# Optimization experiments

Measured on AMD Instinct MI355X. Metric: run time of the kernel, lower is better.

## Reference

```python
import jax, jax.numpy as jnp
import numpy as np

TOPK = 0.1  # fraction of h*w spatial positions, from __init__ default


def setup_inputs() -> dict:
    key = jax.random.key(0)
    x = jax.random.normal(key, (32, 256, 56, 56), dtype=jnp.float32)
    return {"x": x}


def reference(x) -> jnp.ndarray:
    # Faithful translation of TopKLayer.sparse_hw (including its quirky
    # comparison of ascending *ranks* against the spatial *index* of the
    # k-th largest element, exactly as the torch code does).
    n, c, h, w = x.shape
    k = int(max(1, TOPK * h * w))  # topk_keep_num = 313 for 56x56
    x_r = x.reshape(n * c, h * w)              # (nc, hw)
    abs_x = jnp.abs(x_r)
    # ranks[i, j] = ascending rank of abs_x[i, j] within row i
    ranks = jnp.argsort(jnp.argsort(abs_x, axis=1), axis=1)
    # spatial index of the k-th largest |x| in each row
    thr_idx = jax.lax.top_k(abs_x, k)[1][:, -1]  # (nc,)
    mask = (ranks < thr_idx[:, None]).reshape(n, c, h, w)
    return x * mask.astype(x.dtype)
```

## Files before the change

kernel.cpp:

```cpp
#include <hip/hip_runtime.h>
#include <stdint.h>


#define HW    3136
#define NT    256
#define KSEL  313u
#define CAP   320u
#define CAP2  64u
#define M31   0x7fffffffu
#define SENT  0xFFFFFFFFu

#define O_H    0
#define O_CAND 1088
#define O_HC   1408
#define O_TINY 1664
#define LDSW   1728

__device__ __forceinline__ unsigned wscan_incl(unsigned v) {
    const int lane = threadIdx.x & 63;
#pragma unroll
    for (int d = 1; d < 64; d <<= 1) {
        unsigned o = __shfl_up(v, d, 64);
        if (lane >= d) v += o;
    }
    return v;
}

__device__ __forceinline__ unsigned bcast_first(unsigned flag, unsigned val) {
    unsigned long long bal = __ballot(flag != 0);
    if (!bal) return 0u;
    return __shfl(val, __ffsll(bal) - 1, 64);
}

__device__ __forceinline__ void hadd(unsigned* h, unsigned b) {
    const unsigned w = b >> 1;
    atomicAdd(&h[w + (w >> 4)], (b & 1) ? 0x10000u : 1u);
}

template <bool fromTop>
__device__ unsigned wave_finish(unsigned* lds, unsigned m1, unsigned cnt) {
    const int lane = threadIdx.x & 63;
    unsigned* cand = lds + O_CAND;
    unsigned* hc   = lds + O_HC;
    unsigned* tiny = lds + O_TINY;
    if (m1 == 0) return 0u;
    if (cnt > CAP) return SENT;
    for (unsigned i = lane; i < cnt; i += 64) atomicAdd(&hc[cand[i] >> 24], 1u);
    unsigned hh[4];
#pragma unroll
    for (int i = 0; i < 4; ++i) hh[i] = hc[4 * lane + i];
    const unsigned s4 = hh[0] + hh[1] + hh[2] + hh[3];
    unsigned run2 = wscan_incl(s4) - s4;
    unsigned packed2 = 0;
#pragma unroll
    for (int i = 0; i < 4; ++i) {
        if (fromTop) {
            const unsigned suf = cnt - run2 - hh[i];
            if (suf < m1 && m1 <= suf + hh[i])
                packed2 = ((unsigned)(4 * lane + i) << 16) | (m1 - suf);
        } else {
            if (run2 < m1 && m1 <= run2 + hh[i])
                packed2 = ((unsigned)(4 * lane + i) << 16) | (m1 - run2);
        }
        run2 += hh[i];
    }
    packed2 = bcast_first(packed2, packed2);
    if (packed2 == 0) return 0u;
    const unsigned b2 = packed2 >> 16;
    const unsigned m2 = packed2 & 0xFFFFu;
    unsigned tc = 0;
    for (unsigned i = lane; i < cnt; i += 64) tc += ((cand[i] >> 24) == b2);
    const unsigned tincl = wscan_incl(tc);
    const unsigned c2 = __shfl((int)tincl, 63, 64);
    if (c2 > CAP2) return SENT;
    unsigned tpos = tincl - tc;
    for (unsigned i = lane; i < cnt; i += 64) {
        const unsigned cw = cand[i];
        if ((cw >> 24) == b2) tiny[tpos++] = cw;
    }
    unsigned hitf = 0, resv = 0;
    if ((unsigned)lane < c2) {
        const unsigned ci = tiny[lane];
        const unsigned di = fromTop ? (ci ^ 0xFFFu) : ci;
        unsigned r = 1;
        for (unsigned j = 0; j < c2; ++j) {
            const unsigned dj = fromTop ? (tiny[j] ^ 0xFFFu) : tiny[j];
            if (fromTop ? (dj > di) : (dj < di)) r++;
        }
        if (r == m2) { hitf = 1; resv = ci; }
    }
    return bcast_first(hitf, resv);
}

template <bool fromTop>
__device__ void block_fallback(const unsigned* __restrict__ gx,
                               unsigned b0, unsigned m1, unsigned* res) {
    const int t = threadIdx.x;
    for (int j = t; j < HW; j += NT) {
        const unsigned k = gx[j] & M31;
        if ((k >> 20) != b0) continue;
        unsigned Ci = ((k & 0xFFFFFu) << 12) | (unsigned)j;
        if (fromTop) Ci ^= 0xFFFu;
        unsigned r = 1;
        for (int j2 = 0; j2 < HW; ++j2) {
            const unsigned k2 = gx[j2] & M31;
            if ((k2 >> 20) != b0) continue;
            unsigned Cj = ((k2 & 0xFFFFFu) << 12) | (unsigned)j2;
            if (fromTop) Cj ^= 0xFFFu;
            if (fromTop ? (Cj > Ci) : (Cj < Ci)) r++;
        }
        if (r == m1) res[0] = ((k & 0xFFFFFu) << 12) | (unsigned)j;
    }
}

extern "C" __global__ void __launch_bounds__(NT, 6)
topk_kernel(const float* __restrict__ x, float* __restrict__ out) {
    __shared__ unsigned lds[LDSW];
    __shared__ unsigned s_warp[4];
    __shared__ unsigned s_b[4];

    const int t = threadIdx.x;
    const int lane = t & 63;
    const int wid = t >> 6;
    const size_t row = blockIdx.x;
    const uint4* __restrict__ xin = (const uint4*)(x + row * HW);
    uint4* __restrict__ xo = (uint4*)(out + row * HW);
    const unsigned* __restrict__ gx = (const unsigned*)xin;
    const uint4 z4 = make_uint4(0u, 0u, 0u, 0u);
    const bool tail = (t < 16);

    uint4 v0 = xin[t];
    uint4 v1 = xin[t + NT];
    uint4 v2 = xin[t + 2 * NT];
    uint4 vt = tail ? xin[768 + t] : z4;
    asm volatile("" : "+v"(v0.x), "+v"(v0.y), "+v"(v0.z), "+v"(v0.w));
    asm volatile("" : "+v"(v1.x), "+v"(v1.y), "+v"(v1.z), "+v"(v1.w));
    asm volatile("" : "+v"(v2.x), "+v"(v2.y), "+v"(v2.z), "+v"(v2.w));
    asm volatile("" : "+v"(vt.x), "+v"(vt.y), "+v"(vt.z), "+v"(vt.w));

    {
        uint4* h4 = (uint4*)(lds + O_H);
        h4[t] = z4;
        if (tail) h4[NT + t] = z4;
    }
    __syncthreads();

    hadd(lds, (v0.x & M31) >> 20); hadd(lds, (v0.y & M31) >> 20);
    hadd(lds, (v0.z & M31) >> 20); hadd(lds, (v0.w & M31) >> 20);
    hadd(lds, (v1.x & M31) >> 20); hadd(lds, (v1.y & M31) >> 20);
    hadd(lds, (v1.z & M31) >> 20); hadd(lds, (v1.w & M31) >> 20);
    hadd(lds, (v2.x & M31) >> 20); hadd(lds, (v2.y & M31) >> 20);
    hadd(lds, (v2.z & M31) >> 20); hadd(lds, (v2.w & M31) >> 20);
    if (tail) {
        hadd(lds, (vt.x & M31) >> 20); hadd(lds, (vt.y & M31) >> 20);
        hadd(lds, (vt.z & M31) >> 20); hadd(lds, (vt.w & M31) >> 20);
    }
    __syncthreads();

    unsigned cpk[4];
    {
        const unsigned a0 = 4u * (unsigned)t + ((unsigned)t >> 2);
#pragma unroll
        for (int j = 0; j < 4; ++j) cpk[j] = lds[O_H + a0 + j];
    }
    unsigned ssum = 0;
#pragma unroll
    for (int j = 0; j < 4; ++j) ssum += (cpk[j] & 0xFFFFu) + (cpk[j] >> 16);
    const unsigned Si = wscan_incl(ssum);
    if (lane == 63) s_warp[wid] = Si;
    __syncthreads();

    unsigned cross = 0;
    for (int w2 = 0; w2 < wid; ++w2) cross += s_warp[w2];
    const unsigned base = cross + Si - ssum;
    {
        unsigned run = base;
#pragma unroll
        for (int j = 0; j < 4; ++j) {
            const unsigned lo = cpk[j] & 0xFFFFu, hi = cpk[j] >> 16;
            unsigned suf = HW - run - lo;
            if (suf < KSEL && KSEL <= suf + lo) { s_b[0] = 8u * t + 2u * j; s_b[1] = KSEL - suf; }
            run += lo;
            suf = HW - run - hi;
            if (suf < KSEL && KSEL <= suf + hi) { s_b[0] = 8u * t + 2u * j + 1u; s_b[1] = KSEL - suf; }
            run += hi;
        }
    }
    if (t == 0) s_b[3] = 0;
    lds[O_HC + t] = 0;
    __syncthreads();

    auto compact_regs = [&](unsigned b0) {
        auto cput = [&](unsigned wv, unsigned idx) {
            const unsigned k = wv & M31;
            if ((k >> 20) == b0) {
                const unsigned p = atomicAdd(&s_b[3], 1u);
                if (p < CAP) lds[O_CAND + p] = ((k & 0xFFFFFu) << 12) | idx;
            }
        };
        unsigned i0 = 4u * (unsigned)t;
        cput(v0.x, i0); cput(v0.y, i0 + 1u); cput(v0.z, i0 + 2u); cput(v0.w, i0 + 3u);
        i0 = 4u * (unsigned)(t + NT);
        cput(v1.x, i0); cput(v1.y, i0 + 1u); cput(v1.z, i0 + 2u); cput(v1.w, i0 + 3u);
        i0 = 4u * (unsigned)(t + 2 * NT);
        cput(v2.x, i0); cput(v2.y, i0 + 1u); cput(v2.z, i0 + 2u); cput(v2.w, i0 + 3u);
        if (tail) {
            i0 = 4u * (unsigned)(768 + t);
            cput(vt.x, i0); cput(vt.y, i0 + 1u); cput(vt.z, i0 + 2u); cput(vt.w, i0 + 3u);
        }
    };
    const unsigned b0A = s_b[0];
    const unsigned m1A = s_b[1];
    compact_regs(b0A);
    __syncthreads();

    if (wid == 0) {
        const unsigned r = wave_finish<true>(lds, m1A, s_b[3]);
        if (lane == 0) s_b[2] = r;
    }
    __syncthreads();
    unsigned compA = s_b[2];
    if (compA == SENT) {
        block_fallback<true>(gx, b0A, m1A, &s_b[2]);
        __syncthreads();
        compA = s_b[2];
    }
    const unsigned tIdx = compA & 0xFFFu;

    {
        unsigned run = base;
#pragma unroll
        for (int j = 0; j < 4; ++j) {
            const unsigned lo = cpk[j] & 0xFFFFu, hi = cpk[j] >> 16;
            if (run < tIdx && tIdx <= run + lo) { s_b[0] = 8u * t + 2u * j; s_b[1] = tIdx - run; }
            run += lo;
            if (run < tIdx && tIdx <= run + hi) { s_b[0] = 8u * t + 2u * j + 1u; s_b[1] = tIdx - run; }
            run += hi;
        }
    }
    if (t == 0) {
        s_b[3] = 0;
        if (tIdx == 0) { s_b[0] = 0; s_b[1] = 0; }
    }
    lds[O_HC + t] = 0;
    __syncthreads();

    const unsigned b0B = s_b[0];
    const unsigned m1B = s_b[1];
    compact_regs(b0B);
    __syncthreads();

    if (wid == 0) {
        const unsigned r = wave_finish<false>(lds, m1B, s_b[3]);
        if (lane == 0) s_b[2] = r;
    }
    __syncthreads();
    unsigned compB = s_b[2];
    if (compB == SENT) {
        block_fallback<false>(gx, b0B, m1B, &s_b[2]);
        __syncthreads();
        compB = s_b[2];
    }
    const unsigned KB = (b0B << 20) | (compB >> 12);
    const unsigned eB = compB & 0xFFFu;

    {
        auto msk = [&](unsigned wv, unsigned idx) -> unsigned {
            const unsigned k = wv & M31;
            return (k < KB || (k == KB && idx <= eB)) ? wv : 0u;
        };
        uint4 o;
        unsigned i0 = 4u * (unsigned)t;
        o.x = msk(v0.x, i0); o.y = msk(v0.y, i0 + 1u);
        o.z = msk(v0.z, i0 + 2u); o.w = msk(v0.w, i0 + 3u);
        xo[t] = o;
        i0 = 4u * (unsigned)(t + NT);
        o.x = msk(v1.x, i0); o.y = msk(v1.y, i0 + 1u);
        o.z = msk(v1.z, i0 + 2u); o.w = msk(v1.w, i0 + 3u);
        xo[t + NT] = o;
        i0 = 4u * (unsigned)(t + 2 * NT);
        o.x = msk(v2.x, i0); o.y = msk(v2.y, i0 + 1u);
        o.z = msk(v2.z, i0 + 2u); o.w = msk(v2.w, i0 + 3u);
        xo[t + 2 * NT] = o;
        if (tail) {
            i0 = 4u * (unsigned)(768 + t);
            o.x = msk(vt.x, i0); o.y = msk(vt.y, i0 + 1u);
            o.z = msk(vt.z, i0 + 2u); o.w = msk(vt.w, i0 + 3u);
            xo[768 + t] = o;
        }
    }
}

extern "C" void kernel_launch(void* const* d_in, const int* in_sizes, int n_in,
                              void* d_out, int out_size, void* d_ws, size_t ws_size,
                              hipStream_t stream) {
    const float* x = (const float*)d_in[0];
    float* out = (float*)d_out;
    const int rows = in_sizes[0] / HW;
    topk_kernel<<<dim3(rows), dim3(NT), 0, stream>>>(x, out);
}
```

Baseline: 70.04 us.

## Stage row in LDS and halve block size to 128 threads

The block shrinks from 256 to 128 threads, and the whole 3136-element row is copied into shared memory instead of being held in registers. The compaction, fallback and final masking passes then read values from LDS rather than registers or global memory, and the histogram prefix scan now handles 16 bins per thread. The aim is to cut register pressure per thread and keep the fallback path from re-reading global memory. The cost is about 17 KB of LDS per block, fewer waves per block, and extra LDS traffic in every pass, which may reduce latency hiding for a bandwidth-bound kernel.

Result: slower. 74.77 us (+6.8%).

```diff
diff --git a/kernel.cpp b/kernel.cpp
--- a/kernel.cpp
+++ b/kernel.cpp
@@ -3,18 +3,20 @@
 
 
 #define HW    3136
-#define NT    256
+#define NW4   784
+#define NT    128
 #define KSEL  313u
 #define CAP   320u
 #define CAP2  64u
 #define M31   0x7fffffffu
 #define SENT  0xFFFFFFFFu
 
-#define O_H    0
-#define O_CAND 1088
-#define O_HC   1408
-#define O_TINY 1664
-#define LDSW   1728
+#define O_X    0
+#define O_H    3136
+#define O_CAND 3136
+#define O_HC   3520
+#define O_TINY 3776
+#define LDSW   4224
 
 __device__ __forceinline__ unsigned wscan_incl(unsigned v) {
     const int lane = threadIdx.x & 63;
@@ -93,17 +95,17 @@
 }
 
 template <bool fromTop>
-__device__ void block_fallback(const unsigned* __restrict__ gx,
-                               unsigned b0, unsigned m1, unsigned* res) {
+__device__ void block_fallback(const unsigned* sx, unsigned b0, unsigned m1,
+                               unsigned* res) {
     const int t = threadIdx.x;
     for (int j = t; j < HW; j += NT) {
-        const unsigned k = gx[j] & M31;
+        const unsigned k = sx[j] & M31;
         if ((k >> 20) != b0) continue;
         unsigned Ci = ((k & 0xFFFFFu) << 12) | (unsigned)j;
         if (fromTop) Ci ^= 0xFFFu;
         unsigned r = 1;
         for (int j2 = 0; j2 < HW; ++j2) {
-            const unsigned k2 = gx[j2] & M31;
+            const unsigned k2 = sx[j2] & M31;
             if ((k2 >> 20) != b0) continue;
             unsigned Cj = ((k2 & 0xFFFFFu) << 12) | (unsigned)j2;
             if (fromTop) Cj ^= 0xFFFu;
@@ -113,10 +115,10 @@
     }
 }
 
-extern "C" __global__ void __launch_bounds__(NT, 6)
+extern "C" __global__ void __launch_bounds__(NT, 4)
 topk_kernel(const float* __restrict__ x, float* __restrict__ out) {
     __shared__ unsigned lds[LDSW];
-    __shared__ unsigned s_warp[4];
+    __shared__ unsigned s_warp[2];
     __shared__ unsigned s_b[4];
 
     const int t = threadIdx.x;
@@ -125,72 +127,65 @@
     const size_t row = blockIdx.x;
     const uint4* __restrict__ xin = (const uint4*)(x + row * HW);
     uint4* __restrict__ xo = (uint4*)(out + row * HW);
-    const unsigned* __restrict__ gx = (const unsigned*)xin;
+    uint4* s_x4 = (uint4*)(lds + O_X);
+    const unsigned* sx = lds + O_X;
     const uint4 z4 = make_uint4(0u, 0u, 0u, 0u);
     const bool tail = (t < 16);
 
-    uint4 v0 = xin[t];
-    uint4 v1 = xin[t + NT];
-    uint4 v2 = xin[t + 2 * NT];
-    uint4 vt = tail ? xin[768 + t] : z4;
-    asm volatile("" : "+v"(v0.x), "+v"(v0.y), "+v"(v0.z), "+v"(v0.w));
-    asm volatile("" : "+v"(v1.x), "+v"(v1.y), "+v"(v1.z), "+v"(v1.w));
-    asm volatile("" : "+v"(v2.x), "+v"(v2.y), "+v"(v2.z), "+v"(v2.w));
-    asm volatile("" : "+v"(vt.x), "+v"(vt.y), "+v"(vt.z), "+v"(vt.w));
-
     {
         uint4* h4 = (uint4*)(lds + O_H);
-        h4[t] = z4;
-        if (tail) h4[NT + t] = z4;
-    }
-    __syncthreads();
-
-    hadd(lds, (v0.x & M31) >> 20); hadd(lds, (v0.y & M31) >> 20);
-    hadd(lds, (v0.z & M31) >> 20); hadd(lds, (v0.w & M31) >> 20);
-    hadd(lds, (v1.x & M31) >> 20); hadd(lds, (v1.y & M31) >> 20);
-    hadd(lds, (v1.z & M31) >> 20); hadd(lds, (v1.w & M31) >> 20);
-    hadd(lds, (v2.x & M31) >> 20); hadd(lds, (v2.y & M31) >> 20);
-    hadd(lds, (v2.z & M31) >> 20); hadd(lds, (v2.w & M31) >> 20);
+        h4[t] = z4; h4[t + NT] = z4;
+        if (tail) h4[t + 2 * NT] = z4;
+    }
+    __syncthreads();
+
+#pragma unroll
+    for (int i = 0; i < 6; ++i) {
+        const uint4 v = xin[t + NT * i];
+        s_x4[t + NT * i] = v;
+        hadd(lds + O_H, (v.x & M31) >> 20); hadd(lds + O_H, (v.y & M31) >> 20);
+        hadd(lds + O_H, (v.z & M31) >> 20); hadd(lds + O_H, (v.w & M31) >> 20);
+    }
     if (tail) {
-        hadd(lds, (vt.x & M31) >> 20); hadd(lds, (vt.y & M31) >> 20);
-        hadd(lds, (vt.z & M31) >> 20); hadd(lds, (vt.w & M31) >> 20);
-    }
-    __syncthreads();
-
-    unsigned cpk[4];
-    {
-        const unsigned a0 = 4u * (unsigned)t + ((unsigned)t >> 2);
-#pragma unroll
-        for (int j = 0; j < 4; ++j) cpk[j] = lds[O_H + a0 + j];
+        const uint4 v = xin[768 + t];
+        s_x4[768 + t] = v;
+        hadd(lds + O_H, (v.x & M31) >> 20); hadd(lds + O_H, (v.y & M31) >> 20);
+        hadd(lds + O_H, (v.z & M31) >> 20); hadd(lds + O_H, (v.w & M31) >> 20);
+    }
+    __syncthreads();
+
+    unsigned cpk[8];
+    {
+        const unsigned a0 = 8u * (unsigned)t + ((unsigned)t >> 1);
+#pragma unroll
+        for (int j = 0; j < 8; ++j) cpk[j] = lds[O_H + a0 + j];
     }
     unsigned ssum = 0;
 #pragma unroll
-    for (int j = 0; j < 4; ++j) ssum += (cpk[j] & 0xFFFFu) + (cpk[j] >> 16);
+    for (int j = 0; j < 8; ++j) ssum += (cpk[j] & 0xFFFFu) + (cpk[j] >> 16);
     const unsigned Si = wscan_incl(ssum);
     if (lane == 63) s_warp[wid] = Si;
     __syncthreads();
 
-    unsigned cross = 0;
-    for (int w2 = 0; w2 < wid; ++w2) cross += s_warp[w2];
-    const unsigned base = cross + Si - ssum;
+    const unsigned base = (wid ? s_warp[0] : 0u) + Si - ssum;
     {
         unsigned run = base;
 #pragma unroll
-        for (int j = 0; j < 4; ++j) {
+        for (int j = 0; j < 8; ++j) {
             const unsigned lo = cpk[j] & 0xFFFFu, hi = cpk[j] >> 16;
             unsigned suf = HW - run - lo;
-            if (suf < KSEL && KSEL <= suf + lo) { s_b[0] = 8u * t + 2u * j; s_b[1] = KSEL - suf; }
+            if (suf < KSEL && KSEL <= suf + lo) { s_b[0] = 16u * t + 2u * j; s_b[1] = KSEL - suf; }
             run += lo;
             suf = HW - run - hi;
-            if (suf < KSEL && KSEL <= suf + hi) { s_b[0] = 8u * t + 2u * j + 1u; s_b[1] = KSEL - suf; }
+            if (suf < KSEL && KSEL <= suf + hi) { s_b[0] = 16u * t + 2u * j + 1u; s_b[1] = KSEL - suf; }
             run += hi;
         }
     }
     if (t == 0) s_b[3] = 0;
-    lds[O_HC + t] = 0;
-    __syncthreads();
-
-    auto compact_regs = [&](unsigned b0) {
+    lds[O_HC + t] = 0; lds[O_HC + t + NT] = 0;
+    __syncthreads();
+
+    auto compact_lds = [&](unsigned b0) {
         auto cput = [&](unsigned wv, unsigned idx) {
             const unsigned k = wv & M31;
             if ((k >> 20) == b0) {
@@ -198,20 +193,21 @@
                 if (p < CAP) lds[O_CAND + p] = ((k & 0xFFFFFu) << 12) | idx;
             }
         };
-        unsigned i0 = 4u * (unsigned)t;
-        cput(v0.x, i0); cput(v0.y, i0 + 1u); cput(v0.z, i0 + 2u); cput(v0.w, i0 + 3u);
-        i0 = 4u * (unsigned)(t + NT);
-        cput(v1.x, i0); cput(v1.y, i0 + 1u); cput(v1.z, i0 + 2u); cput(v1.w, i0 + 3u);
-        i0 = 4u * (unsigned)(t + 2 * NT);
-        cput(v2.x, i0); cput(v2.y, i0 + 1u); cput(v2.z, i0 + 2u); cput(v2.w, i0 + 3u);
+#pragma unroll
+        for (int i = 0; i < 6; ++i) {
+            const uint4 v = s_x4[t + NT * i];
+            const unsigned i0 = 4u * (unsigned)(t + NT * i);
+            cput(v.x, i0); cput(v.y, i0 + 1u); cput(v.z, i0 + 2u); cput(v.w, i0 + 3u);
+        }
         if (tail) {
-            i0 = 4u * (unsigned)(768 + t);
-            cput(vt.x, i0); cput(vt.y, i0 + 1u); cput(vt.z, i0 + 2u); cput(vt.w, i0 + 3u);
+            const uint4 v = s_x4[768 + t];
+            const unsigned i0 = 4u * (unsigned)(768 + t);
+            cput(v.x, i0); cput(v.y, i0 + 1u); cput(v.z, i0 + 2u); cput(v.w, i0 + 3u);
         }
     };
     const unsigned b0A = s_b[0];
     const unsigned m1A = s_b[1];
-    compact_regs(b0A);
+    compact_lds(b0A);
     __syncthreads();
 
     if (wid == 0) {
@@ -221,7 +217,7 @@
     __syncthreads();
     unsigned compA = s_b[2];
     if (compA == SENT) {
-        block_fallback<true>(gx, b0A, m1A, &s_b[2]);
+        block_fallback<true>(sx, b0A, m1A, &s_b[2]);
         __syncthreads();
         compA = s_b[2];
     }
@@ -230,11 +226,11 @@
     {
         unsigned run = base;
 #pragma unroll
-        for (int j = 0; j < 4; ++j) {
+        for (int j = 0; j < 8; ++j) {
             const unsigned lo = cpk[j] & 0xFFFFu, hi = cpk[j] >> 16;
-            if (run < tIdx && tIdx <= run + lo) { s_b[0] = 8u * t + 2u * j; s_b[1] = tIdx - run; }
+            if (run < tIdx && tIdx <= run + lo) { s_b[0] = 16u * t + 2u * j; s_b[1] = tIdx - run; }
             run += lo;
-            if (run < tIdx && tIdx <= run + hi) { s_b[0] = 8u * t + 2u * j + 1u; s_b[1] = tIdx - run; }
+            if (run < tIdx && tIdx <= run + hi) { s_b[0] = 16u * t + 2u * j + 1u; s_b[1] = tIdx - run; }
             run += hi;
         }
     }
@@ -242,12 +238,12 @@
         s_b[3] = 0;
         if (tIdx == 0) { s_b[0] = 0; s_b[1] = 0; }
     }
-    lds[O_HC + t] = 0;
+    lds[O_HC + t] = 0; lds[O_HC + t + NT] = 0;
     __syncthreads();
 
     const unsigned b0B = s_b[0];
     const unsigned m1B = s_b[1];
-    compact_regs(b0B);
+    compact_lds(b0B);
     __syncthreads();
 
     if (wid == 0) {
@@ -257,7 +253,7 @@
     __syncthreads();
     unsigned compB = s_b[2];
     if (compB == SENT) {
-        block_fallback<false>(gx, b0B, m1B, &s_b[2]);
+        block_fallback<false>(sx, b0B, m1B, &s_b[2]);
         __syncthreads();
         compB = s_b[2];
     }
@@ -269,24 +265,20 @@
             const unsigned k = wv & M31;
             return (k < KB || (k == KB && idx <= eB)) ? wv : 0u;
         };
-        uint4 o;
-        unsigned i0 = 4u * (unsigned)t;
-        o.x = msk(v0.x, i0); o.y = msk(v0.y, i0 + 1u);
-        o.z = msk(v0.z, i0 + 2u); o.w = msk(v0.w, i0 + 3u);
-        xo[t] = o;
-        i0 = 4u * (unsigned)(t + NT);
-        o.x = msk(v1.x, i0); o.y = msk(v1.y, i0 + 1u);
-        o.z = msk(v1.z, i0 + 2u); o.w = msk(v1.w, i0 + 3u);
-        xo[t + NT] = o;
-        i0 = 4u * (unsigned)(t + 2 * NT);
-        o.x = msk(v2.x, i0); o.y = msk(v2.y, i0 + 1u);
-        o.z = msk(v2.z, i0 + 2u); o.w = msk(v2.w, i0 + 3u);
-        xo[t + 2 * NT] = o;
+#pragma unroll
+        for (int i = 0; i < 6; ++i) {
+            uint4 v = s_x4[t + NT * i];
+            const unsigned i0 = 4u * (unsigned)(t + NT * i);
+            v.x = msk(v.x, i0); v.y = msk(v.y, i0 + 1u);
+            v.z = msk(v.z, i0 + 2u); v.w = msk(v.w, i0 + 3u);
+            xo[t + NT * i] = v;
+        }
         if (tail) {
-            i0 = 4u * (unsigned)(768 + t);
-            o.x = msk(vt.x, i0); o.y = msk(vt.y, i0 + 1u);
-            o.z = msk(vt.z, i0 + 2u); o.w = msk(vt.w, i0 + 3u);
-            xo[768 + t] = o;
+            uint4 v = s_x4[768 + t];
+            const unsigned i0 = 4u * (unsigned)(768 + t);
+            v.x = msk(v.x, i0); v.y = msk(v.y, i0 + 1u);
+            v.z = msk(v.z, i0 + 2u); v.w = msk(v.w, i0 + 3u);
+            xo[768 + t] = v;
         }
     }
 }
```
